# Kernel tuning notes

Measured on AMD Instinct MI355X. Metric: run time of the kernel, lower is better.

Reference implementation:

```python
import jax, jax.numpy as jnp
import numpy as np

UNITS = 1024
VOCAB = 50000
EMB = 512
SEQ = 256
BATCH = 256


def setup_inputs() -> dict:
    key = jax.random.key(0)
    ks = jax.random.split(key, 9)
    s = lambda fan_in: 1.0 / np.sqrt(fan_in)
    return {
        "sentences": jax.random.randint(ks[0], (BATCH, SEQ), 0, VOCAB),
        "emb_table": jax.random.normal(ks[1], (VOCAB, EMB), jnp.float32) * 0.05,
        # gate order: i, f, g(cell candidate), o
        "Wx": jax.random.normal(ks[2], (EMB, 4 * UNITS), jnp.float32) * s(EMB),
        "Wh": jax.random.normal(ks[3], (UNITS, 4 * UNITS), jnp.float32) * s(UNITS),
        "b": jnp.zeros((4 * UNITS,), jnp.float32),
        "W1": jax.random.normal(ks[4], (UNITS, 64), jnp.float32) * s(UNITS),
        "b1": jnp.zeros((64,), jnp.float32),
        "W2": jax.random.normal(ks[5], (64, 1), jnp.float32) * s(64),
        "b2": jnp.zeros((1,), jnp.float32),
    }


def _lstm_forward(emb_x, Wx, Wh, b):
    # emb_x: [B, T, E] -> final hidden state [B, U]
    B = emb_x.shape[0]
    U = Wh.shape[0]
    # precompute input projections for all timesteps: [T, B, 4U]
    x_proj = jnp.einsum('bte,eg->tbg', emb_x, Wx) + b

    def step(carry, xp):
        h, c = carry
        gates = xp + h @ Wh  # [B, 4U]
        i, f, g, o = jnp.split(gates, 4, axis=-1)
        i = jax.nn.sigmoid(i)
        f = jax.nn.sigmoid(f)
        g = jnp.tanh(g)
        o = jax.nn.sigmoid(o)
        c = f * c + i * g
        h = o * jnp.tanh(c)
        return (h, c), None

    h0 = jnp.zeros((B, U), emb_x.dtype)
    c0 = jnp.zeros((B, U), emb_x.dtype)
    (h, _), _ = jax.lax.scan(step, (h0, c0), x_proj)
    return h


def reference(sentences, emb_table, Wx, Wh, b, W1, b1, W2, b2):
    emb_x = emb_table[sentences]           # [B, T, E]
    h = _lstm_forward(emb_x, Wx, Wh, b)    # [B, U]
    hidden = h @ W1 + b1                   # Dense(64), linear activation
    logits = hidden @ W2 + b2              # Dense(1)
    return jax.nn.sigmoid(logits)          # [B, 1]
```

## Files before the change

kernel.cpp:

```cpp
#include <hip/hip_runtime.h>

#define B_ 256
#define T_ 256
#define E_ 512
#define U_ 1024
#define G_ 4096
#define V_ 50000
#define TC_ 32
#define NCH_ 8
#define NG_ 8
#define NS_ 32

typedef __bf16 bf16x8 __attribute__((ext_vector_type(8)));
typedef float f32x4 __attribute__((ext_vector_type(4)));
typedef unsigned short us8 __attribute__((ext_vector_type(8)));

__device__ __forceinline__ unsigned short f2bf(float f) {
  union { float f; unsigned u; } v; v.f = f;
  unsigned u = v.u;
  u = (u + 0x7FFFu + ((u >> 16) & 1u)) >> 16;
  return (unsigned short)u;
}
__device__ __forceinline__ float bf2f(unsigned short h) {
  union { unsigned u; float f; } v; v.u = ((unsigned)h) << 16;
  return v.f;
}
__device__ __forceinline__ float sigm_(float x) { return 1.f / (1.f + __expf(-x)); }
__device__ __forceinline__ float tanh_(float x) { return 2.f / (1.f + __expf(-2.f * x)) - 1.f; }

__device__ __forceinline__ void gload16(const void* g, void* l) {
  __builtin_amdgcn_global_load_lds((const __attribute__((address_space(1))) void*)g,
                                   (__attribute__((address_space(3))) void*)l, 16, 0, 0);
}
__device__ __forceinline__ void gload16c(const void* g, void* l) {
  __builtin_amdgcn_global_load_lds((const __attribute__((address_space(1))) void*)g,
                                   (__attribute__((address_space(3))) void*)l, 16, 0, 1);
}

__device__ __forceinline__ int orig_col3(int p) {
  return (((p >> 5) & 3) << 10) + ((p >> 7) << 5) + (p & 31);
}

__global__ void cvt_bf16_kernel(const float* __restrict__ in, unsigned short* __restrict__ out, long n) {
  long i = (((long)blockIdx.x * blockDim.x) + threadIdx.x) << 3;
  long stride = ((long)gridDim.x * blockDim.x) << 3;
  for (; i < n; i += stride) {
    float4 x = *(const float4*)(in + i);
    float4 y = *(const float4*)(in + i + 4);
    us8 v;
    v[0] = f2bf(x.x); v[1] = f2bf(x.y); v[2] = f2bf(x.z); v[3] = f2bf(x.w);
    v[4] = f2bf(y.x); v[5] = f2bf(y.y); v[6] = f2bf(y.z); v[7] = f2bf(y.w);
    *(us8*)(out + i) = v;
  }
}

__global__ void pack_wx_kernel(const float* __restrict__ w, unsigned short* __restrict__ out, int total) {
  int t = blockIdx.x * blockDim.x + threadIdx.x;
  if (t >= total) return;
  int kb = t >> 12, n = t & 4095;
  int oc = orig_col3(n);
  us8 v;
#pragma unroll
  for (int ki = 0; ki < 8; ki++) v[ki] = f2bf(w[(size_t)(kb * 8 + ki) * G_ + oc]);
  *(us8*)(out + (size_t)t * 8) = v;
}

__global__ void pack_wh4_kernel(const float* __restrict__ w, unsigned short* __restrict__ out) {
  int t = blockIdx.x * blockDim.x + threadIdx.x;
  int lane = t & 63;
  int nt  = (t >> 6) & 3;
  int ks  = (t >> 8) & 7;
  int ksl = (t >> 11) & 3;
  int nh  = (t >> 13) & 1;
  int s   = t >> 14;
  int k0 = ksl * 256 + ks * 32 + (lane >> 4) * 8;
  int oc = orig_col3(s * 128 + nh * 64 + nt * 16 + (lane & 15));
  us8 v;
#pragma unroll
  for (int i = 0; i < 8; i++) v[i] = f2bf(w[(size_t)(k0 + i) * G_ + oc]);
  *(us8*)(out + (size_t)t * 8) = v;
}

#define XP_BM 128
#define XP_BN 128
#define XP_KC 64
__global__ __launch_bounds__(256, 2) void xproj_kernel(
    const int* __restrict__ sent, const unsigned short* __restrict__ embb,
    const unsigned short* __restrict__ wxp, const float* __restrict__ bias,
    unsigned short* __restrict__ xp, int t0)
{
  __shared__ __align__(16) unsigned short sA[2][XP_BM * XP_KC];
  __shared__ __align__(16) unsigned short sB[2][XP_KC * XP_BN];
  __shared__ int tok[XP_BM];

  const int tid = threadIdx.x;
  const int lane = tid & 63;
  const int wid = tid >> 6;
  const int m0 = blockIdx.x * XP_BM;
  const int n0 = blockIdx.y * XP_BN;

  if (tid < XP_BM) {
    int row = m0 + tid;
    int tl = row >> 8, b = row & 255;
    tok[tid] = sent[b * T_ + t0 + tl];
  }
  __syncthreads();

  auto stageA = [&](int bf, int kc) {
#pragma unroll
    for (int ii = 0; ii < 4; ii++) {
      int i = wid * 4 + ii;
      int m = i * 8 + (lane >> 3);
      int cl = lane & 7;
      gload16(embb + (size_t)tok[m] * E_ + kc + ((cl ^ (m & 7)) << 3), &sA[bf][i * 512]);
    }
  };
  auto stageB = [&](int bf, int kc) {
    int kb0 = kc >> 3;
#pragma unroll
    for (int jj = 0; jj < 4; jj++) {
      int j = wid * 4 + jj;
      int r = j >> 1;
      int nl = ((j & 1) << 6) + lane;
      int n = nl ^ r;
      gload16(wxp + ((size_t)(kb0 + r) * G_ + n0 + n) * 8, &sB[bf][j * 512]);
    }
  };

  f32x4 acc[4][4];
#pragma unroll
  for (int i = 0; i < 4; i++)
#pragma unroll
    for (int j = 0; j < 4; j++) acc[i][j] = f32x4{0.f, 0.f, 0.f, 0.f};

  const int wm = wid >> 1, wn = wid & 1;

  stageA(0, 0); stageB(0, 0);
  for (int it = 0; it < E_ / XP_KC; it++) {
    int bf = it & 1;
    __syncthreads();
    if (it < E_ / XP_KC - 1) { stageA(bf ^ 1, (it + 1) * XP_KC); stageB(bf ^ 1, (it + 1) * XP_KC); }
#pragma unroll
    for (int kk = 0; kk < 2; kk++) {
      int c = (kk << 2) + (lane >> 4);
      bf16x8 a[4], b[4];
#pragma unroll
      for (int ms = 0; ms < 4; ms++) {
        int m = (wm << 6) + (ms << 4) + (lane & 15);
        a[ms] = *(const bf16x8*)&sA[bf][m * 64 + ((c ^ (m & 7)) << 3)];
      }
#pragma unroll
      for (int ns = 0; ns < 4; ns++) {
        int n = (wn << 6) + (ns << 4) + (lane & 15);
        b[ns] = *(const bf16x8*)&sB[bf][((c << 7) + (n ^ c)) << 3];
      }
#pragma unroll
      for (int ms = 0; ms < 4; ms++)
#pragma unroll
        for (int ns = 0; ns < 4; ns++)
          acc[ms][ns] = __builtin_amdgcn_mfma_f32_16x16x32_bf16(a[ms], b[ns], acc[ms][ns], 0, 0, 0);
    }
  }

#pragma unroll
  for (int ns = 0; ns < 4; ns++) {
    int col = n0 + (wn << 6) + (ns << 4) + (lane & 15);
    float bv = bias[orig_col3(col)];
#pragma unroll
    for (int ms = 0; ms < 4; ms++) {
      int rbase = m0 + (wm << 6) + (ms << 4) + ((lane >> 4) << 2);
#pragma unroll
      for (int rr = 0; rr < 4; rr++)
        xp[(size_t)(rbase + rr) * G_ + col] = f2bf(acc[ms][ns][rr] + bv);
    }
  }
}

__global__ __launch_bounds__(512, 2) void scan_kernel(
    const unsigned short* __restrict__ xpc,
    const unsigned short* __restrict__ whp4,
    unsigned short* __restrict__ hbuf,
    float* __restrict__ cst,
    int* __restrict__ flags,
    int t0)
{
  __shared__ __align__(16) unsigned short sA[32 * 1024];
  __shared__ float sEx[4][32][131];
  __shared__ int sready;

  const int tid = threadIdx.x, lane = tid & 63, w = tid >> 6;
  const int ksl = w & 3, nh = w >> 2;
  const int g = (int)blockIdx.x & 7, s = (int)blockIdx.x >> 3;
  const int m0g = g * 32, u0 = s * 32;
  const int rx = lane & 7, hi = lane >> 4, lo = lane & 15;

  bf16x8 wh[8][4];
  {
    const bf16x8* wb = (const bf16x8*)whp4 + ((((size_t)s * 2 + nh) * 4 + ksl) * 32) * 64;
#pragma unroll
    for (int ks = 0; ks < 8; ks++)
#pragma unroll
      for (int nt = 0; nt < 4; nt++)
        wh[ks][nt] = wb[(ks * 4 + nt) * 64 + lane];
  }

  const int r_e = tid >> 4, ue = (tid & 15) * 2;
  const size_t ci = (size_t)(m0g + r_e) * U_ + u0 + ue;
  float c0v = cst[ci], c1v = cst[ci + 1];

  if (tid == 0) sready = 0;
  __syncthreads();

  for (int ts = 0; ts < TC_; ts++) {
    const int t = t0 + ts;

    const unsigned short* xb = xpc + ((size_t)ts * B_ + (m0g + r_e)) * G_ + s * 128;
    unsigned xiv = *(const unsigned*)(xb + ue);
    unsigned xfv = *(const unsigned*)(xb + 32 + ue);
    unsigned xgv = *(const unsigned*)(xb + 64 + ue);
    unsigned xov = *(const unsigned*)(xb + 96 + ue);

    if (t > 0) {
      if (w == 0) {
        const int* fp = flags + g * 32 + (lane & 31);
        int v, it = 0;
        do { v = __hip_atomic_load(fp, __ATOMIC_RELAXED, __HIP_MEMORY_SCOPE_AGENT); }
        while (__any(v < t) && ++it < (1 << 20));
        if (lane == 0)
          __hip_atomic_store(&sready, t, __ATOMIC_RELAXED, __HIP_MEMORY_SCOPE_WORKGROUP);
      } else {
        int it = 0;
        while (__hip_atomic_load(&sready, __ATOMIC_RELAXED, __HIP_MEMORY_SCOPE_WORKGROUP) < t
               && ++it < (1 << 22)) {}
      }
    }

    const unsigned short* hsrc = hbuf + (size_t)(t & 1) * (B_ * U_) + (size_t)m0g * U_;
#pragma unroll
    for (int jj = 0; jj < 8; jj++) {
      int j = w * 8 + jj;
      int r = j >> 1, k2 = j & 1;
      gload16c(hsrc + (size_t)r * U_ + (((k2 << 6) | (lane ^ (r & 7))) << 3),
               &sA[r * 1024 + k2 * 512]);
    }
    __syncthreads();

    f32x4 acc[2][4];
#pragma unroll
    for (int mt = 0; mt < 2; mt++)
#pragma unroll
      for (int nt = 0; nt < 4; nt++) acc[mt][nt] = f32x4{0.f, 0.f, 0.f, 0.f};
    const char* abase0 = (const char*)sA + (size_t)lo * 2048;
    const char* abase1 = abase0 + 16 * 2048;
#pragma unroll
    for (int ks = 0; ks < 8; ks++) {
      int c = ksl * 32 + ks * 4 + hi;
      int off = (c ^ rx) << 4;
      bf16x8 a0 = *(const bf16x8*)(abase0 + off);
      bf16x8 a1 = *(const bf16x8*)(abase1 + off);
#pragma unroll
      for (int nt = 0; nt < 4; nt++) {
        acc[0][nt] = __builtin_amdgcn_mfma_f32_16x16x32_bf16(a0, wh[ks][nt], acc[0][nt], 0, 0, 0);
        acc[1][nt] = __builtin_amdgcn_mfma_f32_16x16x32_bf16(a1, wh[ks][nt], acc[1][nt], 0, 0, 0);
      }
    }

#pragma unroll
    for (int mt = 0; mt < 2; mt++)
#pragma unroll
      for (int nt = 0; nt < 4; nt++)
#pragma unroll
        for (int rr = 0; rr < 4; rr++)
          sEx[ksl][mt * 16 + hi * 4 + rr][nh * 64 + nt * 16 + lo] = acc[mt][nt][rr];
    __syncthreads();

    {
      float cn[2]; unsigned hv = 0;
#pragma unroll
      for (int j = 0; j < 2; j++) {
        int u = ue + j;
        float gi = sEx[0][r_e][u]      + sEx[1][r_e][u]      + sEx[2][r_e][u]      + sEx[3][r_e][u]      + bf2f((unsigned short)(j ? (xiv >> 16) : xiv));
        float gf = sEx[0][r_e][32 + u] + sEx[1][r_e][32 + u] + sEx[2][r_e][32 + u] + sEx[3][r_e][32 + u] + bf2f((unsigned short)(j ? (xfv >> 16) : xfv));
        float gg = sEx[0][r_e][64 + u] + sEx[1][r_e][64 + u] + sEx[2][r_e][64 + u] + sEx[3][r_e][64 + u] + bf2f((unsigned short)(j ? (xgv >> 16) : xgv));
        float go = sEx[0][r_e][96 + u] + sEx[1][r_e][96 + u] + sEx[2][r_e][96 + u] + sEx[3][r_e][96 + u] + bf2f((unsigned short)(j ? (xov >> 16) : xov));
        float co = j ? c1v : c0v;
        float cv = sigm_(gf) * co + sigm_(gi) * tanh_(gg);
        cn[j] = cv;
        hv |= (unsigned)f2bf(sigm_(go) * tanh_(cv)) << (16 * j);
      }
      c0v = cn[0]; c1v = cn[1];
      *(unsigned*)(hbuf + (size_t)((t + 1) & 1) * (B_ * U_) + ci) = hv;
    }
    __syncthreads();
    if (tid == 0)
      __hip_atomic_store(flags + g * 32 + s, t + 1, __ATOMIC_RELAXED, __HIP_MEMORY_SCOPE_AGENT);
  }

  cst[ci] = c0v; cst[ci + 1] = c1v;
}

__global__ __launch_bounds__(256) void dense_kernel(
    const unsigned short* __restrict__ h, const float* __restrict__ W1, const float* __restrict__ b1,
    const float* __restrict__ W2, const float* __restrict__ b2, float* __restrict__ out)
{
  int tid = threadIdx.x, j = tid & 63, kq = tid >> 6;
  const unsigned short* hr = h + (size_t)blockIdx.x * U_;
  float s = 0.f;
#pragma unroll 8
  for (int k = kq * 256; k < kq * 256 + 256; k++) s += bf2f(hr[k]) * W1[k * 64 + j];
  __shared__ float red[4][64];
  red[kq][j] = s;
  __syncthreads();
  if (tid < 64) {
    float hid = red[0][j] + red[1][j] + red[2][j] + red[3][j] + b1[j];
    float p = hid * W2[j];
#pragma unroll
    for (int off = 32; off; off >>= 1) p += __shfl_down(p, off, 64);
    if (j == 0) out[blockIdx.x] = 1.f / (1.f + __expf(-(p + b2[0])));
  }
}

extern "C" void kernel_launch(void* const* d_in, const int* in_sizes, int n_in,
                              void* d_out, int out_size, void* d_ws, size_t ws_size,
                              hipStream_t stream) {
  const int*   sent = (const int*)d_in[0];
  const float* emb  = (const float*)d_in[1];
  const float* Wx   = (const float*)d_in[2];
  const float* Wh   = (const float*)d_in[3];
  const float* bias = (const float*)d_in[4];
  const float* W1   = (const float*)d_in[5];
  const float* b1   = (const float*)d_in[6];
  const float* W2   = (const float*)d_in[7];
  const float* b2   = (const float*)d_in[8];
  float* out = (float*)d_out;

  char* ws = (char*)d_ws;
  size_t off = 0;
  auto alloc = [&](size_t bytes) { void* p = ws + off; off += (bytes + 255) & ~(size_t)255; return p; };
  unsigned short* embb = (unsigned short*)alloc((size_t)V_ * E_ * 2);
  unsigned short* wxp  = (unsigned short*)alloc((size_t)E_ * G_ * 2);
  unsigned short* whp4 = (unsigned short*)alloc((size_t)U_ * G_ * 2);
  unsigned short* xpc  = (unsigned short*)alloc((size_t)TC_ * B_ * G_ * 2);
  unsigned short* hbuf = (unsigned short*)alloc((size_t)2 * B_ * U_ * 2);
  float*          cst  = (float*)alloc((size_t)B_ * U_ * 4);
  int*            flg  = (int*)alloc((size_t)NG_ * 32 * 4);

  hipLaunchKernelGGL(cvt_bf16_kernel, dim3(12500), dim3(256), 0, stream, emb, embb, (long)V_ * E_);
  hipLaunchKernelGGL(pack_wx_kernel, dim3((E_ / 8) * G_ / 256), dim3(256), 0, stream, Wx, wxp, (E_ / 8) * G_);
  hipLaunchKernelGGL(pack_wh4_kernel, dim3(2048), dim3(256), 0, stream, Wh, whp4);
  hipMemsetAsync(hbuf, 0, (size_t)B_ * U_ * 2, stream);
  hipMemsetAsync(cst, 0, (size_t)B_ * U_ * 4, stream);
  hipMemsetAsync(flg, 0, (size_t)NG_ * 32 * 4, stream);

  for (int ch = 0; ch < NCH_; ch++) {
    hipLaunchKernelGGL(xproj_kernel, dim3(TC_ * B_ / XP_BM, G_ / XP_BN), dim3(256), 0, stream,
                       sent, embb, wxp, bias, xpc, ch * TC_);
    hipLaunchKernelGGL(scan_kernel, dim3(NG_ * NS_), dim3(512), 0, stream,
                       xpc, whp4, hbuf, cst, flg, ch * TC_);
  }
  hipLaunchKernelGGL(dense_kernel, dim3(B_), dim3(256), 0, stream,
                     hbuf , W1, b1, W2, b2, out);
}
```

Baseline: 1.508 ms.

## Rewrite input-projection GEMM with 256x256 tiles and triple-buffered async loads

Replaces the 128x128, double-buffered xproj kernel with a 512-thread, 256x256-tile kernel. It uses a K-step of 32, a three-stage LDS ring with explicit vmcnt waits and one barrier per step, and interleaves the next-tile loads between MFMA groups under raised s_setprio. The goal is better operand reuse and hiding of global-load latency in the embedding-gather GEMM that runs before each scan chunk. The cost is higher register and LDS use at one block per CU, and only 32x16 blocks per launch, so occupancy and load balance could suffer.

```diff
diff --git a/kernel.cpp b/kernel.cpp
--- a/kernel.cpp
+++ b/kernel.cpp
@@ -81,97 +81,109 @@
   *(us8*)(out + (size_t)t * 8) = v;
 }
 
-#define XP_BM 128
-#define XP_BN 128
-#define XP_KC 64
-__global__ __launch_bounds__(256, 2) void xproj_kernel(
+__global__ __launch_bounds__(512, 1) void xproj8_kernel(
     const int* __restrict__ sent, const unsigned short* __restrict__ embb,
     const unsigned short* __restrict__ wxp, const float* __restrict__ bias,
     unsigned short* __restrict__ xp, int t0)
 {
-  __shared__ __align__(16) unsigned short sA[2][XP_BM * XP_KC];
-  __shared__ __align__(16) unsigned short sB[2][XP_KC * XP_BN];
-  __shared__ int tok[XP_BM];
-
-  const int tid = threadIdx.x;
-  const int lane = tid & 63;
-  const int wid = tid >> 6;
-  const int m0 = blockIdx.x * XP_BM;
-  const int n0 = blockIdx.y * XP_BN;
-
-  if (tid < XP_BM) {
-    int row = m0 + tid;
-    int tl = row >> 8, b = row & 255;
-    tok[tid] = sent[b * T_ + t0 + tl];
+  __shared__ __align__(16) unsigned short sAx[3 * 8192];
+  __shared__ __align__(16) unsigned short sBx[3 * 8192];
+  __shared__ int tok[256];
+
+  const int tid = threadIdx.x, lane = tid & 63, w = tid >> 6;
+  const int wm = w >> 2, wn = w & 3;
+  const int m0 = blockIdx.x * 256, n0 = blockIdx.y * 256;
+
+  for (int i = tid; i < 256; i += 512) {
+    int row = m0 + i;
+    tok[i] = sent[(row & 255) * T_ + t0 + (row >> 8)];
   }
   __syncthreads();
 
-  auto stageA = [&](int bf, int kc) {
-#pragma unroll
-    for (int ii = 0; ii < 4; ii++) {
-      int i = wid * 4 + ii;
-      int m = i * 8 + (lane >> 3);
-      int cl = lane & 7;
-      gload16(embb + (size_t)tok[m] * E_ + kc + ((cl ^ (m & 7)) << 3), &sA[bf][i * 512]);
-    }
+  const int swz = (((lane & 3) ^ ((lane >> 2) & 3)) << 3);
+  const int r0 = w * 32 + (lane >> 2);
+  const unsigned short* a0src = embb + (size_t)tok[r0] * E_ + swz;
+  const unsigned short* a1src = embb + (size_t)tok[r0 + 16] * E_ + swz;
+  const unsigned short* b0src = wxp + (((size_t)((w * 2 + 0) >> 2)) * G_ + n0 + ((w * 2 + 0) & 3) * 64 + lane) * 8;
+  const unsigned short* b1src = wxp + (((size_t)((w * 2 + 1) >> 2)) * G_ + n0 + ((w * 2 + 1) & 3) * 64 + lane) * 8;
+
+  unsigned short* aDst0 = &sAx[(w * 2 + 0) * 512];
+  unsigned short* aDst1 = &sAx[(w * 2 + 1) * 512];
+  unsigned short* bDst0 = &sBx[(w * 2 + 0) * 512];
+  unsigned short* bDst1 = &sBx[(w * 2 + 1) * 512];
+
+  const unsigned short* aRd = sAx + (wm * 128 + (lane & 15)) * 32 + (((lane >> 4) ^ (lane & 3)) << 3);
+  const unsigned short* bRd = sBx + ((((lane >> 4)) << 8) + wn * 64 + (lane & 15)) * 8;
+
+  f32x4 acc[8][4];
+#pragma unroll
+  for (int i = 0; i < 8; i++)
+#pragma unroll
+    for (int j = 0; j < 4; j++) acc[i][j] = f32x4{0.f, 0.f, 0.f, 0.f};
+
+  auto stageA = [&](int kt) {
+    int b = kt % 3;
+    gload16(a0src + kt * 32, aDst0 + b * 8192);
+    gload16(a1src + kt * 32, aDst1 + b * 8192);
   };
-  auto stageB = [&](int bf, int kc) {
-    int kb0 = kc >> 3;
-#pragma unroll
-    for (int jj = 0; jj < 4; jj++) {
-      int j = wid * 4 + jj;
-      int r = j >> 1;
-      int nl = ((j & 1) << 6) + lane;
-      int n = nl ^ r;
-      gload16(wxp + ((size_t)(kb0 + r) * G_ + n0 + n) * 8, &sB[bf][j * 512]);
-    }
+  auto stageB = [&](int kt) {
+    int b = kt % 3;
+    gload16(b0src + (size_t)kt * (4 * G_ * 8), bDst0 + b * 8192);
+    gload16(b1src + (size_t)kt * (4 * G_ * 8), bDst1 + b * 8192);
   };
 
-  f32x4 acc[4][4];
-#pragma unroll
-  for (int i = 0; i < 4; i++)
-#pragma unroll
-    for (int j = 0; j < 4; j++) acc[i][j] = f32x4{0.f, 0.f, 0.f, 0.f};
-
-  const int wm = wid >> 1, wn = wid & 1;
-
-  stageA(0, 0); stageB(0, 0);
-  for (int it = 0; it < E_ / XP_KC; it++) {
-    int bf = it & 1;
-    __syncthreads();
-    if (it < E_ / XP_KC - 1) { stageA(bf ^ 1, (it + 1) * XP_KC); stageB(bf ^ 1, (it + 1) * XP_KC); }
-#pragma unroll
-    for (int kk = 0; kk < 2; kk++) {
-      int c = (kk << 2) + (lane >> 4);
-      bf16x8 a[4], b[4];
-#pragma unroll
-      for (int ms = 0; ms < 4; ms++) {
-        int m = (wm << 6) + (ms << 4) + (lane & 15);
-        a[ms] = *(const bf16x8*)&sA[bf][m * 64 + ((c ^ (m & 7)) << 3)];
-      }
-#pragma unroll
-      for (int ns = 0; ns < 4; ns++) {
-        int n = (wn << 6) + (ns << 4) + (lane & 15);
-        b[ns] = *(const bf16x8*)&sB[bf][((c << 7) + (n ^ c)) << 3];
-      }
-#pragma unroll
-      for (int ms = 0; ms < 4; ms++)
-#pragma unroll
-        for (int ns = 0; ns < 4; ns++)
-          acc[ms][ns] = __builtin_amdgcn_mfma_f32_16x16x32_bf16(a[ms], b[ns], acc[ms][ns], 0, 0, 0);
-    }
-  }
-
-#pragma unroll
-  for (int ns = 0; ns < 4; ns++) {
-    int col = n0 + (wn << 6) + (ns << 4) + (lane & 15);
+  stageA(0); stageB(0); stageA(1);
+
+  for (int kt = 0; kt < 16; ++kt) {
+    const int buf = kt % 3;
+    if (kt == 15) { asm volatile("s_waitcnt vmcnt(0)" ::: "memory"); }
+    else          { asm volatile("s_waitcnt vmcnt(2)" ::: "memory"); }
+    __builtin_amdgcn_s_barrier();
+
+    const unsigned short* aB = aRd + buf * 8192;
+    const unsigned short* bB = bRd + buf * 8192;
+    bf16x8 b0 = *(const bf16x8*)(bB);
+    bf16x8 b1 = *(const bf16x8*)(bB + 128);
+    bf16x8 b2 = *(const bf16x8*)(bB + 256);
+    bf16x8 b3 = *(const bf16x8*)(bB + 384);
+
+    if (kt < 15) stageB(kt + 1);
+
+    __builtin_amdgcn_s_setprio(1);
+#pragma unroll
+    for (int mf = 0; mf < 4; mf++) {
+      bf16x8 a = *(const bf16x8*)(aB + mf * 512);
+      acc[mf][0] = __builtin_amdgcn_mfma_f32_16x16x32_bf16(a, b0, acc[mf][0], 0, 0, 0);
+      acc[mf][1] = __builtin_amdgcn_mfma_f32_16x16x32_bf16(a, b1, acc[mf][1], 0, 0, 0);
+      acc[mf][2] = __builtin_amdgcn_mfma_f32_16x16x32_bf16(a, b2, acc[mf][2], 0, 0, 0);
+      acc[mf][3] = __builtin_amdgcn_mfma_f32_16x16x32_bf16(a, b3, acc[mf][3], 0, 0, 0);
+    }
+    __builtin_amdgcn_s_setprio(0);
+
+    if (kt < 14) stageA(kt + 2);
+
+    __builtin_amdgcn_s_setprio(1);
+#pragma unroll
+    for (int mf = 4; mf < 8; mf++) {
+      bf16x8 a = *(const bf16x8*)(aB + mf * 512);
+      acc[mf][0] = __builtin_amdgcn_mfma_f32_16x16x32_bf16(a, b0, acc[mf][0], 0, 0, 0);
+      acc[mf][1] = __builtin_amdgcn_mfma_f32_16x16x32_bf16(a, b1, acc[mf][1], 0, 0, 0);
+      acc[mf][2] = __builtin_amdgcn_mfma_f32_16x16x32_bf16(a, b2, acc[mf][2], 0, 0, 0);
+      acc[mf][3] = __builtin_amdgcn_mfma_f32_16x16x32_bf16(a, b3, acc[mf][3], 0, 0, 0);
+    }
+    __builtin_amdgcn_s_setprio(0);
+  }
+
+#pragma unroll
+  for (int nf = 0; nf < 4; nf++) {
+    int col = n0 + wn * 64 + nf * 16 + (lane & 15);
     float bv = bias[orig_col3(col)];
 #pragma unroll
-    for (int ms = 0; ms < 4; ms++) {
-      int rbase = m0 + (wm << 6) + (ms << 4) + ((lane >> 4) << 2);
+    for (int mf = 0; mf < 8; mf++) {
+      int rb = m0 + wm * 128 + mf * 16 + ((lane >> 4) << 2);
 #pragma unroll
       for (int rr = 0; rr < 4; rr++)
-        xp[(size_t)(rbase + rr) * G_ + col] = f2bf(acc[ms][ns][rr] + bv);
+        xp[(size_t)(rb + rr) * G_ + col] = f2bf(acc[mf][nf][rr] + bv);
     }
   }
 }
@@ -353,7 +365,7 @@
   hipMemsetAsync(flg, 0, (size_t)NG_ * 32 * 4, stream);
 
   for (int ch = 0; ch < NCH_; ch++) {
-    hipLaunchKernelGGL(xproj_kernel, dim3(TC_ * B_ / XP_BM, G_ / XP_BN), dim3(256), 0, stream,
+    hipLaunchKernelGGL(xproj8_kernel, dim3(TC_ * B_ / 256, G_ / 256), dim3(512), 0, stream,
                        sent, embb, wxp, bias, xpc, ch * TC_);
     hipLaunchKernelGGL(scan_kernel, dim3(NG_ * NS_), dim3(512), 0, stream,
                        xpc, whp4, hbuf, cst, flg, ch * TC_);
```

New measurement: 1.593 ms. 5.7% more time.
